# Performance work log

Hardware: AMD Instinct MI355X
Metric: run time of the kernel (lower is better)

## Reference

```python
import jax, jax.numpy as jnp
import numpy as np

D = 768  # input_hidden_dim
H = 768  # TGLU_hidden_dim
E = 128  # num_entity
B = 32   # batch_size
S = 128  # max_seq_len
LN_EPS = 1e-5


def setup_inputs() -> dict:
    key = jax.random.key(0)
    ks = jax.random.split(key, 14)
    sc = 1.0 / np.sqrt(D)
    return {
        "entity_text_cls": jax.random.normal(ks[0], (E, D), jnp.float32),
        "entity_text_tokens": jax.random.normal(ks[1], (E, S, D), jnp.float32),
        "mention_text_cls": jax.random.normal(ks[2], (B, D), jnp.float32),
        "mention_text_tokens": jax.random.normal(ks[3], (B, S, D), jnp.float32),
        "Wq": jax.random.normal(ks[4], (D, H), jnp.float32) * sc,
        "bq": jax.random.normal(ks[5], (H,), jnp.float32) * 0.02,
        "Wk": jax.random.normal(ks[6], (D, H), jnp.float32) * sc,
        "bk": jax.random.normal(ks[7], (H,), jnp.float32) * 0.02,
        "Wv": jax.random.normal(ks[8], (D, H), jnp.float32) * sc,
        "bv": jax.random.normal(ks[9], (H,), jnp.float32) * 0.02,
        "Wc": jax.random.normal(ks[10], (D, H), jnp.float32) * sc,
        "bc": jax.random.normal(ks[11], (H,), jnp.float32) * 0.02,
        "ln_g": jnp.ones((H,), jnp.float32),
        "ln_b": jnp.zeros((H,), jnp.float32),
    }


def reference(entity_text_cls, entity_text_tokens, mention_text_cls, mention_text_tokens,
              Wq, bq, Wk, bk, Wv, bv, Wc, bc, ln_g, ln_b):
    # projections
    cls_fc = entity_text_cls @ Wc + bc                     # [E, H]
    q = entity_text_tokens @ Wq + bq                       # [E, S, H]
    k = mention_text_tokens @ Wk + bk                      # [B, S, H]
    v = mention_text_tokens @ Wv + bv                      # [B, S, H]
    # broadcast cross attention: every entity attends to every mention
    scale = 1.0 / jnp.sqrt(jnp.asarray(H, q.dtype))
    scores = jnp.einsum('esh,bth->ebst', q, k) * scale     # [E, B, S, S]
    probs = jax.nn.softmax(scores, axis=-1)                # [E, B, S, S]
    # context = mean over query positions of probs @ v  -> fuse mean into einsum
    seq = jnp.asarray(q.shape[1], q.dtype)
    ctx = jnp.einsum('ebst,bth->ebh', probs, v) / seq      # [E, B, H]
    # layernorm over H
    mu = jnp.mean(ctx, axis=-1, keepdims=True)
    var = jnp.mean(jnp.square(ctx - mu), axis=-1, keepdims=True)
    ctx_ln = (ctx - mu) * jax.lax.rsqrt(var + LN_EPS) * ln_g + ln_b
    # dual matching scores
    g2l = jnp.einsum('eh,ebh->eb', cls_fc, ctx_ln).T       # [B, E]
    g2g = mention_text_cls @ entity_text_cls.T             # [B, E]
    return (g2l + g2g) * 0.5
```

## Files before the change

### kernel.cpp

```cpp
#include <hip/hip_runtime.h>

typedef unsigned short u16;
typedef __bf16 bf16x8 __attribute__((ext_vector_type(8)));
typedef float f32x4 __attribute__((ext_vector_type(4)));
typedef u16 u16x8 __attribute__((ext_vector_type(8)));
typedef u16 u16x4 __attribute__((ext_vector_type(4)));

static __device__ __forceinline__ u16 f2bf(float x){
  unsigned u = __float_as_uint(x);
  u += 0x7fffu + ((u >> 16) & 1u);
  return (u16)(u >> 16);
}
static __device__ __forceinline__ float bf2f(u16 u){
  return __uint_as_float(((unsigned)u) << 16);
}

#define MFMA __builtin_amdgcn_mfma_f32_16x16x32_bf16

__global__ __launch_bounds__(256) void prep(
    const float* __restrict__ s0, u16* __restrict__ d0,
    const float* __restrict__ s1, u16* __restrict__ d1,
    const float* __restrict__ s2, u16* __restrict__ d2,
    const float* __restrict__ s3, u16* __restrict__ d3,
    const float* __restrict__ w0, const float* __restrict__ w1,
    const float* __restrict__ w2, u16* __restrict__ e0,
    u16* __restrict__ e1, u16* __restrict__ e2)
{
  int blk = blockIdx.x;
  if (blk < 8016){
    int i = blk * 256 + threadIdx.x;
    const float* s; u16* d; int off;
    if (i < 1572864)      { s=s0; d=d0; off=i; }
    else if (i < 1966080) { s=s1; d=d1; off=i-1572864; }
    else if (i < 1978368) { s=s2; d=d2; off=i-1966080; }
    else                  { s=s3; d=d3; off=i-1978368; }
    const float4* s4 = (const float4*)s;
    float4 a = s4[(size_t)off*2], b = s4[(size_t)off*2+1];
    u16x8 r;
    r[0]=f2bf(a.x); r[1]=f2bf(a.y); r[2]=f2bf(a.z); r[3]=f2bf(a.w);
    r[4]=f2bf(b.x); r[5]=f2bf(b.y); r[6]=f2bf(b.z); r[7]=f2bf(b.w);
    *(u16x8*)(d + (size_t)off*8) = r;
  } else {
    int n = blk - 8016;
    int z = n / 576, rem = n % 576;
    const float* s = (z==0) ? w0 : (z==1) ? w1 : w2;
    u16*         d = (z==0) ? e0 : (z==1) ? e1 : e2;
    __shared__ float t[32][33];
    int bx = (rem % 24) * 32, by = (rem / 24) * 32;
    int tx = threadIdx.x & 31, ty = (threadIdx.x >> 5) * 4;
    for (int i=0;i<4;i++)
      t[ty+i][tx] = s[(size_t)(by+ty+i)*768 + bx+tx];
    __syncthreads();
    for (int i=0;i<4;i++)
      d[(size_t)(bx+ty+i)*768 + by+tx] = f2bf(t[tx][ty+i]);
  }
}

#define DECL_ACC \
  f32x4 acc00={},acc01={},acc02={},acc03={}, \
        acc10={},acc11={},acc12={},acc13={}, \
        acc20={},acc21={},acc22={},acc23={}, \
        acc30={},acc31={},acc32={},acc33={};

#define GLD1(GP, LP) __builtin_amdgcn_global_load_lds( \
    (const __attribute__((address_space(1))) unsigned int*)(GP), \
    (__attribute__((address_space(3))) unsigned int*)(LP), 16, 0, 0)

#define CORE_SETUP \
  int tid = threadIdx.x; \
  int lane = tid & 63, w = tid >> 6; \
  int wm = (w >> 1) * 64, wn = (w & 1) * 64; \
  int quad = lane >> 4, l16 = lane & 15; \
  int r8 = lane >> 3, c8 = lane & 7; \
  int p0 = quad ^ (l16 & 7); \
  const u16* Agl = Ablk + (size_t)(w*32 + r8)*KS + (size_t)((c8 ^ r8)*8); \
  const u16* Bgl = Bblk + (size_t)(w*32 + r8)*KS + (size_t)((c8 ^ r8)*8); \
  u16* sAl = sA + w*2048; \
  u16* sBl = sB + w*2048; \
  const u16* paA0 = sA + (wm + l16)*64 + p0*8; \
  const u16* paA1 = sA + (wm + l16)*64 + (p0^4)*8; \
  const u16* paB0 = sB + (wn + l16)*64 + p0*8; \
  const u16* paB1 = sB + (wn + l16)*64 + (p0^4)*8;

#define GLDS8(K0) do { \
  const u16* ga_ = Agl + (K0); \
  const u16* gb_ = Bgl + (K0); \
  GLD1(ga_,         sAl);        GLD1(ga_ +  8*KS, sAl +  512); \
  GLD1(ga_ + 16*KS, sAl + 1024); GLD1(ga_ + 24*KS, sAl + 1536); \
  GLD1(gb_,         sBl);        GLD1(gb_ +  8*KS, sBl +  512); \
  GLD1(gb_ + 16*KS, sBl + 1024); GLD1(gb_ + 24*KS, sBl + 1536); \
} while(0)

#define KKSTEP(PA, PB) do { \
  bf16x8 a0 = *(const bf16x8*)(PA); \
  bf16x8 a1 = *(const bf16x8*)((PA) + 1024); \
  bf16x8 a2 = *(const bf16x8*)((PA) + 2048); \
  bf16x8 a3 = *(const bf16x8*)((PA) + 3072); \
  bf16x8 b0 = *(const bf16x8*)(PB); \
  bf16x8 b1 = *(const bf16x8*)((PB) + 1024); \
  bf16x8 b2 = *(const bf16x8*)((PB) + 2048); \
  bf16x8 b3 = *(const bf16x8*)((PB) + 3072); \
  acc00 = MFMA(a0,b0,acc00,0,0,0); acc01 = MFMA(a0,b1,acc01,0,0,0); \
  acc02 = MFMA(a0,b2,acc02,0,0,0); acc03 = MFMA(a0,b3,acc03,0,0,0); \
  acc10 = MFMA(a1,b0,acc10,0,0,0); acc11 = MFMA(a1,b1,acc11,0,0,0); \
  acc12 = MFMA(a1,b2,acc12,0,0,0); acc13 = MFMA(a1,b3,acc13,0,0,0); \
  acc20 = MFMA(a2,b0,acc20,0,0,0); acc21 = MFMA(a2,b1,acc21,0,0,0); \
  acc22 = MFMA(a2,b2,acc22,0,0,0); acc23 = MFMA(a2,b3,acc23,0,0,0); \
  acc30 = MFMA(a3,b0,acc30,0,0,0); acc31 = MFMA(a3,b1,acc31,0,0,0); \
  acc32 = MFMA(a3,b2,acc32,0,0,0); acc33 = MFMA(a3,b3,acc33,0,0,0); \
} while(0)

#define KLOOP do { \
  for (int k0 = 0; k0 < KLEN; k0 += 64){ \
    __syncthreads(); \
    GLDS8(k0); \
    __syncthreads(); \
    KKSTEP(paA0, paB0); \
    KKSTEP(paA1, paB1); \
  } } while(0)

template<int KLEN, int KS, bool TRANSC>
static __device__ __forceinline__ void gemm128_core(
    const u16* __restrict__ Ablk, const u16* __restrict__ Bblk,
    const float* __restrict__ bias, u16* __restrict__ C,
    int mb, int nb, u16* sA, u16* sB)
{
  CORE_SETUP
  DECL_ACC
  KLOOP;
  int cb = nb*128 + wn + l16;
  float bb0=0.f, bb1=0.f, bb2=0.f, bb3=0.f;
  if (bias){ bb0=bias[cb]; bb1=bias[cb+16]; bb2=bias[cb+32]; bb3=bias[cb+48]; }
  if constexpr (!TRANSC) {
#define GEPI(IM,A0,A1,A2,A3) do { \
  int r0_ = mb*128 + wm + (IM)*16 + quad*4; \
  _Pragma("unroll") \
  for (int j=0;j<4;j++){ \
    C[(size_t)(r0_+j)*768 + cb     ] = f2bf(A0[j]+bb0); \
    C[(size_t)(r0_+j)*768 + cb + 16] = f2bf(A1[j]+bb1); \
    C[(size_t)(r0_+j)*768 + cb + 32] = f2bf(A2[j]+bb2); \
    C[(size_t)(r0_+j)*768 + cb + 48] = f2bf(A3[j]+bb3); \
  } } while(0)
    GEPI(0, acc00,acc01,acc02,acc03);
    GEPI(1, acc10,acc11,acc12,acc13);
    GEPI(2, acc20,acc21,acc22,acc23);
    GEPI(3, acc30,acc31,acc32,acc33);
#undef GEPI
  } else {
#define GEPT(IM,A0,A1,A2,A3) do { \
  int t0_ = wm + (IM)*16 + quad*4; \
  u16x4 p0 = {f2bf(A0[0]+bb0),f2bf(A0[1]+bb0),f2bf(A0[2]+bb0),f2bf(A0[3]+bb0)}; \
  u16x4 p1 = {f2bf(A1[0]+bb1),f2bf(A1[1]+bb1),f2bf(A1[2]+bb1),f2bf(A1[3]+bb1)}; \
  u16x4 p2 = {f2bf(A2[0]+bb2),f2bf(A2[1]+bb2),f2bf(A2[2]+bb2),f2bf(A2[3]+bb2)}; \
  u16x4 p3 = {f2bf(A3[0]+bb3),f2bf(A3[1]+bb3),f2bf(A3[2]+bb3),f2bf(A3[3]+bb3)}; \
  *(u16x4*)(C + (size_t)(cb     )*128 + t0_) = p0; \
  *(u16x4*)(C + (size_t)(cb + 16)*128 + t0_) = p1; \
  *(u16x4*)(C + (size_t)(cb + 32)*128 + t0_) = p2; \
  *(u16x4*)(C + (size_t)(cb + 48)*128 + t0_) = p3; \
} while(0)
    GEPT(0, acc00,acc01,acc02,acc03);
    GEPT(1, acc10,acc11,acc12,acc13);
    GEPT(2, acc20,acc21,acc22,acc23);
    GEPT(3, acc30,acc31,acc32,acc33);
#undef GEPT
  }
}

__global__ __launch_bounds__(256, 1) void gemm_kvc(
    const u16* __restrict__ men, const u16* __restrict__ eclsb,
    const u16* __restrict__ wkt, const u16* __restrict__ wvt,
    const u16* __restrict__ wct,
    const float* __restrict__ bk, const float* __restrict__ bv,
    const float* __restrict__ bc,
    u16* __restrict__ k2b, u16* __restrict__ vtb, u16* __restrict__ clsb)
{
  __shared__ __align__(16) u16 sA[128*64];
  __shared__ __align__(16) u16 sB[128*64];
  int y = blockIdx.y, mb = blockIdx.x;
  if (y < 6){
    gemm128_core<768,768,false>(men + (size_t)mb*128*768, wkt + (size_t)y*128*768,
                                bk, k2b, mb, y, sA, sB);
  } else if (y < 12){
    gemm128_core<768,768,true>(men + (size_t)mb*128*768, wvt + (size_t)(y-6)*128*768,
                               bv, vtb + (size_t)mb*98304, mb, y-6, sA, sB);
  } else {
    if (mb >= 6) return;
    gemm128_core<768,768,false>(eclsb, wct + (size_t)mb*128*768, bc, clsb, 0, mb, sA, sB);
  }
}

__global__ __launch_bounds__(256, 1) void gemm_g(
    const u16* __restrict__ k2b, const u16* __restrict__ wqb,
    const float* __restrict__ bq, u16* __restrict__ gtb,
    float* __restrict__ rbias)
{
  __shared__ __align__(16) u16 sA[128*64];
  __shared__ __align__(16) u16 sB[128*64];
  int y = blockIdx.y, mb = blockIdx.x;
  if (y < 6){
    gemm128_core<768,768,false>(k2b + (size_t)mb*128*768,
                                wqb + (size_t)y*128*768,
                                nullptr, gtb, mb, y, sA, sB);
  } else {
    int tid = threadIdx.x;
    int rr = tid >> 1, half = (tid & 1) * 384;
    int row = mb*128 + rr;
    const u16* p = k2b + (size_t)row*768 + half;
    const float* q = bq + half;
    float s = 0.f;
    #pragma unroll
    for (int i=0;i<48;i++){
      u16x8 v = *(const u16x8*)(p + i*8);
      s += bf2f(v[0])*q[i*8]   + bf2f(v[1])*q[i*8+1]
         + bf2f(v[2])*q[i*8+2] + bf2f(v[3])*q[i*8+3]
         + bf2f(v[4])*q[i*8+4] + bf2f(v[5])*q[i*8+5]
         + bf2f(v[6])*q[i*8+6] + bf2f(v[7])*q[i*8+7];
    }
    s += __shfl_xor(s, 1);
    if ((tid & 1) == 0) rbias[row] = s;
  }
}

__global__ __launch_bounds__(256, 1) void ctx2(
    const u16* __restrict__ ptbf, const u16* __restrict__ vtb,
    u16* __restrict__ ctxb)
{
  __shared__ __align__(16) u16 sA[128*64];
  __shared__ __align__(16) u16 sB[128*64];
  int b = blockIdx.y, nb = blockIdx.x;
  gemm128_core<128,128,false>(ptbf + (size_t)b*16384,
                              vtb + (size_t)b*98304 + (size_t)nb*16384,
                              nullptr, ctxb + (size_t)b*98304, 0, nb, sA, sB);
}

__global__ __launch_bounds__(256, 1) void attnk(
    const u16* __restrict__ ent, const u16* __restrict__ gt,
    const float* __restrict__ rbias, u16* __restrict__ ptbf)
{
  __shared__ __align__(16) u16 sA[128*64];
  __shared__ __align__(16) u16 sB[128*64];
  __shared__ float rbufA[256];
  __shared__ float rbufB[256];
  int bi = blockIdx.x;
  int b = bi >> 7, e = bi & 127;
  const u16* Ablk = ent + (size_t)e * 128 * 768;
  const u16* Bblk = gt  + (size_t)b * 128 * 768;
  constexpr int KLEN = 768, KS = 768;
  CORE_SETUP
  DECL_ACC
  KLOOP;
  const float c1 = 0.036084391824351615f * 1.4426950408889634f;
  float rs0 = rbias[b*128 + wn      + l16] * c1;
  float rs1 = rbias[b*128 + wn + 16 + l16] * c1;
  float rs2 = rbias[b*128 + wn + 32 + l16] * c1;
  float rs3 = rbias[b*128 + wn + 48 + l16] * c1;
#define EXPSUM(IM,A0,A1,A2,A3) do { \
  _Pragma("unroll") \
  for (int j=0;j<4;j++){ \
    int r_ = wm + (IM)*16 + quad*4 + j; \
    float e0 = exp2f(fmaf(A0[j], c1, rs0)); \
    float e1 = exp2f(fmaf(A1[j], c1, rs1)); \
    float e2 = exp2f(fmaf(A2[j], c1, rs2)); \
    float e3 = exp2f(fmaf(A3[j], c1, rs3)); \
    A0[j]=e0; A1[j]=e1; A2[j]=e2; A3[j]=e3; \
    float s = (e0+e1)+(e2+e3); \
    s += __shfl_xor(s,1); s += __shfl_xor(s,2); \
    s += __shfl_xor(s,4); s += __shfl_xor(s,8); \
    if (l16==0) rbufB[(w&1)*128 + r_] = s; \
  } } while(0)
  EXPSUM(0, acc00,acc01,acc02,acc03);
  EXPSUM(1, acc10,acc11,acc12,acc13);
  EXPSUM(2, acc20,acc21,acc22,acc23);
  EXPSUM(3, acc30,acc31,acc32,acc33);
#undef EXPSUM
  __syncthreads();
  float csum0=0.f, csum1=0.f, csum2=0.f, csum3=0.f;
#define CSUM(IM,A0,A1,A2,A3) do { \
  _Pragma("unroll") \
  for (int j=0;j<4;j++){ \
    int r_ = wm + (IM)*16 + quad*4 + j; \
    float inv = __builtin_amdgcn_rcpf(rbufB[r_]+rbufB[128+r_]); \
    csum0 += A0[j]*inv; csum1 += A1[j]*inv; \
    csum2 += A2[j]*inv; csum3 += A3[j]*inv; \
  } } while(0)
  CSUM(0, acc00,acc01,acc02,acc03);
  CSUM(1, acc10,acc11,acc12,acc13);
  CSUM(2, acc20,acc21,acc22,acc23);
  CSUM(3, acc30,acc31,acc32,acc33);
#undef CSUM
  csum0 += __shfl_xor(csum0,16); csum0 += __shfl_xor(csum0,32);
  csum1 += __shfl_xor(csum1,16); csum1 += __shfl_xor(csum1,32);
  csum2 += __shfl_xor(csum2,16); csum2 += __shfl_xor(csum2,32);
  csum3 += __shfl_xor(csum3,16); csum3 += __shfl_xor(csum3,32);
  if (quad == 0){
    rbufA[(w>>1)*128 + wn      + l16] = csum0;
    rbufA[(w>>1)*128 + wn + 16 + l16] = csum1;
    rbufA[(w>>1)*128 + wn + 32 + l16] = csum2;
    rbufA[(w>>1)*128 + wn + 48 + l16] = csum3;
  }
  __syncthreads();
  if (tid < 128)
    ptbf[((size_t)b*128 + e)*128 + tid] =
        f2bf((rbufA[tid] + rbufA[128+tid]) * 0.0078125f);
}

__global__ __launch_bounds__(256) void fin(
    const u16* __restrict__ ctxb, const u16* __restrict__ clsfc,
    const float* __restrict__ ecls, const float* __restrict__ mcls,
    const float* __restrict__ lng, const float* __restrict__ lnb,
    float* __restrict__ out)
{
  int bi = blockIdx.x;
  int b = bi >> 7, e = bi & 127;
  int tid = threadIdx.x;
  int lane = tid & 63, w = tid >> 6;
  __shared__ float redbuf[8];
  const u16* cr = ctxb + ((size_t)b*128 + e)*768;
  float a0 = bf2f(cr[tid]), a1 = bf2f(cr[tid+256]), a2 = bf2f(cr[tid+512]);
  float s1 = a0+a1+a2;
  float s2 = a0*a0 + a1*a1 + a2*a2;
  #pragma unroll
  for (int d2=1; d2<64; d2<<=1){ s1 += __shfl_xor(s1,d2); s2 += __shfl_xor(s2,d2); }
  if (lane==0){ redbuf[w]=s1; redbuf[4+w]=s2; }
  __syncthreads();
  s1 = redbuf[0]+redbuf[1]+redbuf[2]+redbuf[3];
  s2 = redbuf[4]+redbuf[5]+redbuf[6]+redbuf[7];
  float mu = s1 * (1.0f/768.0f);
  float var = s2 * (1.0f/768.0f) - mu*mu;
  float rstd = rsqrtf(var + 1e-5f);
  float dd = 0.f;
  {
    int h = tid;
    float y = (a0-mu)*rstd*lng[h] + lnb[h];
    dd += y * bf2f(clsfc[e*768+h]) + mcls[b*768+h]*ecls[e*768+h];
    h = tid + 256;
    y = (a1-mu)*rstd*lng[h] + lnb[h];
    dd += y * bf2f(clsfc[e*768+h]) + mcls[b*768+h]*ecls[e*768+h];
    h = tid + 512;
    y = (a2-mu)*rstd*lng[h] + lnb[h];
    dd += y * bf2f(clsfc[e*768+h]) + mcls[b*768+h]*ecls[e*768+h];
  }
  #pragma unroll
  for (int d2=1; d2<64; d2<<=1) dd += __shfl_xor(dd,d2);
  __syncthreads();
  if (lane==0) redbuf[w] = dd;
  __syncthreads();
  if (tid==0) out[bi] = 0.5f * (redbuf[0]+redbuf[1]+redbuf[2]+redbuf[3]);
}

extern "C" void kernel_launch(void* const* d_in, const int* in_sizes, int n_in,
                              void* d_out, int out_size, void* d_ws, size_t ws_size,
                              hipStream_t stream)
{
  (void)in_sizes; (void)n_in; (void)out_size; (void)ws_size;
  const float* ecls = (const float*)d_in[0];
  const float* etok = (const float*)d_in[1];
  const float* mcls = (const float*)d_in[2];
  const float* mtok = (const float*)d_in[3];
  const float* Wq   = (const float*)d_in[4];
  const float* bq   = (const float*)d_in[5];
  const float* Wk   = (const float*)d_in[6];
  const float* bk   = (const float*)d_in[7];
  const float* Wv   = (const float*)d_in[8];
  const float* bv   = (const float*)d_in[9];
  const float* Wc   = (const float*)d_in[10];
  const float* bc   = (const float*)d_in[11];
  const float* lng  = (const float*)d_in[12];
  const float* lnb  = (const float*)d_in[13];
  float* out = (float*)d_out;
  char* ws = (char*)d_ws;

  u16* ent_bf  = (u16*)(ws + 0);
  u16* men_bf  = (u16*)(ws + 25165824);
  u16* ecls_bf = (u16*)(ws + 31457280);
  u16* wq_bf   = (u16*)(ws + 31653888);
  u16* wkt     = (u16*)(ws + 32833536);
  u16* wvt     = (u16*)(ws + 34013184);
  u16* wct     = (u16*)(ws + 35192832);
  u16* k2b     = (u16*)(ws + 36372480);
  u16* vtb     = (u16*)(ws + 42663936);
  u16* clsb    = (u16*)(ws + 48955392);
  u16* gtb     = (u16*)(ws + 49152000);
  float* rbias = (float*)(ws + 55443456);
  u16* ptbf    = (u16*)(ws + 55459840);
  u16* ctxb    = (u16*)(ws + 56508416);

  prep<<<9744, 256, 0, stream>>>(etok, ent_bf, mtok, men_bf,
                                 ecls, ecls_bf, Wq, wq_bf,
                                 Wk, Wv, Wc, wkt, wvt, wct);
  gemm_kvc<<<dim3(32,13), 256, 0, stream>>>(men_bf, ecls_bf, wkt, wvt, wct,
                                            bk, bv, bc, k2b, vtb, clsb);
  gemm_g<<<dim3(32,7), 256, 0, stream>>>(k2b, wq_bf, bq, gtb, rbias);
  attnk<<<4096, 256, 0, stream>>>(ent_bf, gtb, rbias, ptbf);
  ctx2<<<dim3(6,32), 256, 0, stream>>>(ptbf, vtb, ctxb);
  fin<<<4096, 256, 0, stream>>>(ctxb, clsb, ecls, mcls, lng, lnb, out);
}
```

Measured before the change: 304.9 us.

## Precompute Wk·WqT product to drop K projection, widen attention tile

Folds the Q/K projections algebraically. A small 768x768 product M = Wq·Wkᵀ is computed in the prep kernel, so the mention-side G = men·Mᵀ + bias is built in one GEMM, and the separate K GEMM and its launch go away. The row-bias terms are rewritten as precomputed weight-bias dot products. The attention kernel now processes 256 entity rows (two entities) per block against 128 mention positions. It normalises softmax per row with in-register shuffles instead of shared-memory round trips, halving the grid. This adds register pressure (32 accumulators per wave) and a bf16 rounding of the fused weight product.

```diff
diff --git a/kernel.cpp b/kernel.cpp
--- a/kernel.cpp
+++ b/kernel.cpp
@@ -17,54 +17,15 @@
 
 #define MFMA __builtin_amdgcn_mfma_f32_16x16x32_bf16
 
-__global__ __launch_bounds__(256) void prep(
-    const float* __restrict__ s0, u16* __restrict__ d0,
-    const float* __restrict__ s1, u16* __restrict__ d1,
-    const float* __restrict__ s2, u16* __restrict__ d2,
-    const float* __restrict__ s3, u16* __restrict__ d3,
-    const float* __restrict__ w0, const float* __restrict__ w1,
-    const float* __restrict__ w2, u16* __restrict__ e0,
-    u16* __restrict__ e1, u16* __restrict__ e2)
-{
-  int blk = blockIdx.x;
-  if (blk < 8016){
-    int i = blk * 256 + threadIdx.x;
-    const float* s; u16* d; int off;
-    if (i < 1572864)      { s=s0; d=d0; off=i; }
-    else if (i < 1966080) { s=s1; d=d1; off=i-1572864; }
-    else if (i < 1978368) { s=s2; d=d2; off=i-1966080; }
-    else                  { s=s3; d=d3; off=i-1978368; }
-    const float4* s4 = (const float4*)s;
-    float4 a = s4[(size_t)off*2], b = s4[(size_t)off*2+1];
-    u16x8 r;
-    r[0]=f2bf(a.x); r[1]=f2bf(a.y); r[2]=f2bf(a.z); r[3]=f2bf(a.w);
-    r[4]=f2bf(b.x); r[5]=f2bf(b.y); r[6]=f2bf(b.z); r[7]=f2bf(b.w);
-    *(u16x8*)(d + (size_t)off*8) = r;
-  } else {
-    int n = blk - 8016;
-    int z = n / 576, rem = n % 576;
-    const float* s = (z==0) ? w0 : (z==1) ? w1 : w2;
-    u16*         d = (z==0) ? e0 : (z==1) ? e1 : e2;
-    __shared__ float t[32][33];
-    int bx = (rem % 24) * 32, by = (rem / 24) * 32;
-    int tx = threadIdx.x & 31, ty = (threadIdx.x >> 5) * 4;
-    for (int i=0;i<4;i++)
-      t[ty+i][tx] = s[(size_t)(by+ty+i)*768 + bx+tx];
-    __syncthreads();
-    for (int i=0;i<4;i++)
-      d[(size_t)(bx+ty+i)*768 + by+tx] = f2bf(t[tx][ty+i]);
-  }
-}
+#define GLD1(GP, LP) __builtin_amdgcn_global_load_lds( \
+    (const __attribute__((address_space(1))) unsigned int*)(GP), \
+    (__attribute__((address_space(3))) unsigned int*)(LP), 16, 0, 0)
 
 #define DECL_ACC \
   f32x4 acc00={},acc01={},acc02={},acc03={}, \
         acc10={},acc11={},acc12={},acc13={}, \
         acc20={},acc21={},acc22={},acc23={}, \
         acc30={},acc31={},acc32={},acc33={};
-
-#define GLD1(GP, LP) __builtin_amdgcn_global_load_lds( \
-    (const __attribute__((address_space(1))) unsigned int*)(GP), \
-    (__attribute__((address_space(3))) unsigned int*)(LP), 16, 0, 0)
 
 #define CORE_SETUP \
   int tid = threadIdx.x; \
@@ -149,14 +110,14 @@
   } else {
 #define GEPT(IM,A0,A1,A2,A3) do { \
   int t0_ = wm + (IM)*16 + quad*4; \
-  u16x4 p0 = {f2bf(A0[0]+bb0),f2bf(A0[1]+bb0),f2bf(A0[2]+bb0),f2bf(A0[3]+bb0)}; \
-  u16x4 p1 = {f2bf(A1[0]+bb1),f2bf(A1[1]+bb1),f2bf(A1[2]+bb1),f2bf(A1[3]+bb1)}; \
-  u16x4 p2 = {f2bf(A2[0]+bb2),f2bf(A2[1]+bb2),f2bf(A2[2]+bb2),f2bf(A2[3]+bb2)}; \
-  u16x4 p3 = {f2bf(A3[0]+bb3),f2bf(A3[1]+bb3),f2bf(A3[2]+bb3),f2bf(A3[3]+bb3)}; \
-  *(u16x4*)(C + (size_t)(cb     )*128 + t0_) = p0; \
-  *(u16x4*)(C + (size_t)(cb + 16)*128 + t0_) = p1; \
-  *(u16x4*)(C + (size_t)(cb + 32)*128 + t0_) = p2; \
-  *(u16x4*)(C + (size_t)(cb + 48)*128 + t0_) = p3; \
+  u16x4 p0_ = {f2bf(A0[0]+bb0),f2bf(A0[1]+bb0),f2bf(A0[2]+bb0),f2bf(A0[3]+bb0)}; \
+  u16x4 p1_ = {f2bf(A1[0]+bb1),f2bf(A1[1]+bb1),f2bf(A1[2]+bb1),f2bf(A1[3]+bb1)}; \
+  u16x4 p2_ = {f2bf(A2[0]+bb2),f2bf(A2[1]+bb2),f2bf(A2[2]+bb2),f2bf(A2[3]+bb2)}; \
+  u16x4 p3_ = {f2bf(A3[0]+bb3),f2bf(A3[1]+bb3),f2bf(A3[2]+bb3),f2bf(A3[3]+bb3)}; \
+  *(u16x4*)(C + (size_t)(cb     )*128 + t0_) = p0_; \
+  *(u16x4*)(C + (size_t)(cb + 16)*128 + t0_) = p1_; \
+  *(u16x4*)(C + (size_t)(cb + 32)*128 + t0_) = p2_; \
+  *(u16x4*)(C + (size_t)(cb + 48)*128 + t0_) = p3_; \
 } while(0)
     GEPT(0, acc00,acc01,acc02,acc03);
     GEPT(1, acc10,acc11,acc12,acc13);
@@ -166,49 +127,162 @@
   }
 }
 
-__global__ __launch_bounds__(256, 1) void gemm_kvc(
+__global__ __launch_bounds__(256) void prep(
+    const float* __restrict__ etok, u16* __restrict__ entb,
+    const float* __restrict__ mtok, u16* __restrict__ menb,
+    const float* __restrict__ ecls, u16* __restrict__ eclsb,
+    const float* __restrict__ Wv, const float* __restrict__ Wc,
+    u16* __restrict__ wvt, u16* __restrict__ wct,
+    const float* __restrict__ Wq, const float* __restrict__ Wk,
+    u16* __restrict__ mtb,
+    const float* __restrict__ bq, const float* __restrict__ bk,
+    float* __restrict__ wrb, float* __restrict__ c2b)
+{
+  __shared__ __align__(16) u16 shm[2*128*72];
+  int blk = blockIdx.x;
+  int tid = threadIdx.x;
+  if (blk < 7728){
+    int i = blk * 256 + tid;
+    const float* s; u16* d; int off;
+    if (i < 1572864)      { s=etok; d=entb; off=i; }
+    else if (i < 1966080) { s=mtok; d=menb; off=i-1572864; }
+    else                  { s=ecls; d=eclsb; off=i-1966080; }
+    const float4* s4 = (const float4*)s;
+    float4 a = s4[(size_t)off*2], b = s4[(size_t)off*2+1];
+    u16x8 r;
+    r[0]=f2bf(a.x); r[1]=f2bf(a.y); r[2]=f2bf(a.z); r[3]=f2bf(a.w);
+    r[4]=f2bf(b.x); r[5]=f2bf(b.y); r[6]=f2bf(b.z); r[7]=f2bf(b.w);
+    *(u16x8*)(d + (size_t)off*8) = r;
+  } else if (blk < 8880){
+    int n = blk - 7728;
+    int z = n / 576, rem = n % 576;
+    const float* s = z ? Wc : Wv;
+    u16*         d = z ? wct : wvt;
+    float* t = (float*)shm;
+    int bx = (rem % 24) * 32, by = (rem / 24) * 32;
+    int tx = tid & 31, ty = (tid >> 5) * 4;
+    for (int i=0;i<4;i++)
+      t[(ty+i)*33 + tx] = s[(size_t)(by+ty+i)*768 + bx+tx];
+    __syncthreads();
+    for (int i=0;i<4;i++)
+      d[(size_t)(bx+ty+i)*768 + by+tx] = f2bf(t[tx*33 + ty+i]);
+  } else if (blk < 8916){
+    int n = blk - 8880; int mbq = n/6, nbq = n%6;
+    u16* tA = shm; u16* tB = shm + 128*72;
+    int lane = tid & 63, w = tid >> 6;
+    int wm = (w >> 1) * 64, wn = (w & 1) * 64;
+    int quad = lane >> 4, l16 = lane & 15;
+    int sr = tid >> 3, sc = (tid & 7) * 8;
+    const float* Ag = Wq + (size_t)(mbq*128+sr)*768 + sc;
+    const float* Bg = Wk + (size_t)(nbq*128+sr)*768 + sc;
+    u16* tAp = tA + sr*72 + sc;
+    u16* tBp = tB + sr*72 + sc;
+    DECL_ACC
+    for (int k0=0;k0<768;k0+=64){
+      __syncthreads();
+#define STG(G) do { \
+      float4 xa0=*(const float4*)(Ag+(G)*32*768+k0), xa1=*(const float4*)(Ag+(G)*32*768+k0+4); \
+      float4 xb0=*(const float4*)(Bg+(G)*32*768+k0), xb1=*(const float4*)(Bg+(G)*32*768+k0+4); \
+      u16x8 ra={f2bf(xa0.x),f2bf(xa0.y),f2bf(xa0.z),f2bf(xa0.w), \
+                f2bf(xa1.x),f2bf(xa1.y),f2bf(xa1.z),f2bf(xa1.w)}; \
+      u16x8 rb={f2bf(xb0.x),f2bf(xb0.y),f2bf(xb0.z),f2bf(xb0.w), \
+                f2bf(xb1.x),f2bf(xb1.y),f2bf(xb1.z),f2bf(xb1.w)}; \
+      *(u16x8*)(tAp+(G)*32*72)=ra; *(u16x8*)(tBp+(G)*32*72)=rb; \
+      } while(0)
+      STG(0); STG(1); STG(2); STG(3);
+#undef STG
+      __syncthreads();
+#define KK72(KB) do { \
+      const u16* pa_=tA+(wm+l16)*72+(KB)+quad*8; \
+      const u16* pb_=tB+(wn+l16)*72+(KB)+quad*8; \
+      bf16x8 a0=*(const bf16x8*)(pa_),      a1=*(const bf16x8*)(pa_+16*72); \
+      bf16x8 a2=*(const bf16x8*)(pa_+32*72),a3=*(const bf16x8*)(pa_+48*72); \
+      bf16x8 b0=*(const bf16x8*)(pb_),      b1=*(const bf16x8*)(pb_+16*72); \
+      bf16x8 b2=*(const bf16x8*)(pb_+32*72),b3=*(const bf16x8*)(pb_+48*72); \
+      acc00=MFMA(a0,b0,acc00,0,0,0); acc01=MFMA(a0,b1,acc01,0,0,0); \
+      acc02=MFMA(a0,b2,acc02,0,0,0); acc03=MFMA(a0,b3,acc03,0,0,0); \
+      acc10=MFMA(a1,b0,acc10,0,0,0); acc11=MFMA(a1,b1,acc11,0,0,0); \
+      acc12=MFMA(a1,b2,acc12,0,0,0); acc13=MFMA(a1,b3,acc13,0,0,0); \
+      acc20=MFMA(a2,b0,acc20,0,0,0); acc21=MFMA(a2,b1,acc21,0,0,0); \
+      acc22=MFMA(a2,b2,acc22,0,0,0); acc23=MFMA(a2,b3,acc23,0,0,0); \
+      acc30=MFMA(a3,b0,acc30,0,0,0); acc31=MFMA(a3,b1,acc31,0,0,0); \
+      acc32=MFMA(a3,b2,acc32,0,0,0); acc33=MFMA(a3,b3,acc33,0,0,0); \
+      } while(0)
+      KK72(0); KK72(32);
+#undef KK72
+    }
+    int cb = nbq*128 + wn + l16;
+#define GEPM(IM,A0,A1,A2,A3) do { \
+    int r0_ = mbq*128 + wm + (IM)*16 + quad*4; \
+    _Pragma("unroll") \
+    for (int j=0;j<4;j++){ \
+      mtb[(size_t)(r0_+j)*768 + cb     ] = f2bf(A0[j]); \
+      mtb[(size_t)(r0_+j)*768 + cb + 16] = f2bf(A1[j]); \
+      mtb[(size_t)(r0_+j)*768 + cb + 32] = f2bf(A2[j]); \
+      mtb[(size_t)(r0_+j)*768 + cb + 48] = f2bf(A3[j]); \
+    } } while(0)
+    GEPM(0, acc00,acc01,acc02,acc03);
+    GEPM(1, acc10,acc11,acc12,acc13);
+    GEPM(2, acc20,acc21,acc22,acc23);
+    GEPM(3, acc30,acc31,acc32,acc33);
+#undef GEPM
+  } else if (blk < 8928){
+    int n = blk - 8916;
+    const float* M; const float* v; float* o;
+    int j;
+    if (n < 6){ M=Wk; v=bq; o=wrb; j=n; } else { M=Wq; v=bk; o=c2b; j=n-6; }
+    int rr = tid >> 1, row = j*128 + rr;
+    const float4* p = (const float4*)(M + (size_t)row*768 + (tid&1)*384);
+    const float4* q = (const float4*)(v + (tid&1)*384);
+    float s = 0.f;
+    #pragma unroll 8
+    for (int i=0;i<96;i++){
+      float4 a=p[i], c=q[i];
+      s += a.x*c.x + a.y*c.y + a.z*c.z + a.w*c.w;
+    }
+    s += __shfl_xor(s, 1);
+    if (!(tid&1)) o[row] = s;
+  } else {
+    float s = 0.f;
+    for (int i=tid;i<768;i+=256) s += bk[i]*bq[i];
+    #pragma unroll
+    for (int d2=1; d2<64; d2<<=1) s += __shfl_xor(s,d2);
+    float* red = (float*)shm;
+    int lane = tid & 63, w = tid >> 6;
+    if (lane==0) red[w]=s;
+    __syncthreads();
+    if (tid==0) wrb[768] = red[0]+red[1]+red[2]+red[3];
+  }
+}
+
+__global__ __launch_bounds__(256, 1) void proj(
     const u16* __restrict__ men, const u16* __restrict__ eclsb,
-    const u16* __restrict__ wkt, const u16* __restrict__ wvt,
-    const u16* __restrict__ wct,
-    const float* __restrict__ bk, const float* __restrict__ bv,
-    const float* __restrict__ bc,
-    u16* __restrict__ k2b, u16* __restrict__ vtb, u16* __restrict__ clsb)
+    const u16* __restrict__ wvt, const u16* __restrict__ wct,
+    const u16* __restrict__ mtb,
+    const float* __restrict__ bv, const float* __restrict__ bc,
+    const float* __restrict__ c2b, const float* __restrict__ wrb,
+    u16* __restrict__ vtb, u16* __restrict__ gtb, u16* __restrict__ clsb,
+    float* __restrict__ rbias)
 {
   __shared__ __align__(16) u16 sA[128*64];
   __shared__ __align__(16) u16 sB[128*64];
   int y = blockIdx.y, mb = blockIdx.x;
   if (y < 6){
-    gemm128_core<768,768,false>(men + (size_t)mb*128*768, wkt + (size_t)y*128*768,
-                                bk, k2b, mb, y, sA, sB);
+    gemm128_core<768,768,true>(men + (size_t)mb*128*768, wvt + (size_t)y*128*768,
+                               bv, vtb + (size_t)mb*98304, mb, y, sA, sB);
   } else if (y < 12){
-    gemm128_core<768,768,true>(men + (size_t)mb*128*768, wvt + (size_t)(y-6)*128*768,
-                               bv, vtb + (size_t)mb*98304, mb, y-6, sA, sB);
-  } else {
+    gemm128_core<768,768,false>(men + (size_t)mb*128*768, mtb + (size_t)(y-6)*128*768,
+                                c2b, gtb, mb, y-6, sA, sB);
+  } else if (y == 12){
     if (mb >= 6) return;
     gemm128_core<768,768,false>(eclsb, wct + (size_t)mb*128*768, bc, clsb, 0, mb, sA, sB);
-  }
-}
-
-__global__ __launch_bounds__(256, 1) void gemm_g(
-    const u16* __restrict__ k2b, const u16* __restrict__ wqb,
-    const float* __restrict__ bq, u16* __restrict__ gtb,
-    float* __restrict__ rbias)
-{
-  __shared__ __align__(16) u16 sA[128*64];
-  __shared__ __align__(16) u16 sB[128*64];
-  int y = blockIdx.y, mb = blockIdx.x;
-  if (y < 6){
-    gemm128_core<768,768,false>(k2b + (size_t)mb*128*768,
-                                wqb + (size_t)y*128*768,
-                                nullptr, gtb, mb, y, sA, sB);
   } else {
     int tid = threadIdx.x;
-    int rr = tid >> 1, half = (tid & 1) * 384;
-    int row = mb*128 + rr;
-    const u16* p = k2b + (size_t)row*768 + half;
-    const float* q = bq + half;
+    int rr = tid >> 1, row = mb*128 + rr;
+    const u16* p = men + (size_t)row*768 + (tid&1)*384;
+    const float* q = wrb + (tid&1)*384;
     float s = 0.f;
-    #pragma unroll
+    #pragma unroll 8
     for (int i=0;i<48;i++){
       u16x8 v = *(const u16x8*)(p + i*8);
       s += bf2f(v[0])*q[i*8]   + bf2f(v[1])*q[i*8+1]
@@ -217,7 +291,145 @@
          + bf2f(v[6])*q[i*8+6] + bf2f(v[7])*q[i*8+7];
     }
     s += __shfl_xor(s, 1);
-    if ((tid & 1) == 0) rbias[row] = s;
+    if (!(tid&1)) rbias[row] = s + wrb[768];
+  }
+}
+
+__global__ __launch_bounds__(256, 1) void attnk(
+    const u16* __restrict__ ent, const u16* __restrict__ gt,
+    const float* __restrict__ rbias, u16* __restrict__ ptbf)
+{
+  __shared__ __align__(16) u16 sA[256*64];
+  __shared__ __align__(16) u16 sB[128*64];
+  __shared__ float rbuf[512];
+  int bi = blockIdx.x;
+  int b = bi >> 6, ep = bi & 63;
+  const u16* Ablk = ent + (size_t)ep * 256 * 768;
+  const u16* Bblk = gt  + (size_t)b * 128 * 768;
+  int tid = threadIdx.x;
+  int lane = tid & 63, w = tid >> 6;
+  int quad = lane >> 4, l16 = lane & 15;
+  int r8 = lane >> 3, c8 = lane & 7;
+  int p0 = quad ^ (l16 & 7);
+  const u16* Agl = Ablk + (size_t)(w*64 + r8)*768 + (size_t)((c8 ^ r8)*8);
+  const u16* Bgl = Bblk + (size_t)(w*32 + r8)*768 + (size_t)((c8 ^ r8)*8);
+  u16* sAl = sA + w*4096;
+  u16* sBl = sB + w*2048;
+  const u16* paA0 = sA + (w*64 + l16)*64 + p0*8;
+  const u16* paA1 = sA + (w*64 + l16)*64 + (p0^4)*8;
+  const u16* paB0 = sB + l16*64 + p0*8;
+  const u16* paB1 = sB + l16*64 + (p0^4)*8;
+  f32x4 acc00={},acc01={},acc02={},acc03={},acc04={},acc05={},acc06={},acc07={},
+        acc10={},acc11={},acc12={},acc13={},acc14={},acc15={},acc16={},acc17={},
+        acc20={},acc21={},acc22={},acc23={},acc24={},acc25={},acc26={},acc27={},
+        acc30={},acc31={},acc32={},acc33={},acc34={},acc35={},acc36={},acc37={};
+#define AKH(PA, PB) do { \
+  bf16x8 b0 = *(const bf16x8*)(PB); \
+  bf16x8 b1 = *(const bf16x8*)((PB) + 1024); \
+  bf16x8 b2 = *(const bf16x8*)((PB) + 2048); \
+  bf16x8 b3 = *(const bf16x8*)((PB) + 3072); \
+  bf16x8 b4 = *(const bf16x8*)((PB) + 4096); \
+  bf16x8 b5 = *(const bf16x8*)((PB) + 5120); \
+  bf16x8 b6 = *(const bf16x8*)((PB) + 6144); \
+  bf16x8 b7 = *(const bf16x8*)((PB) + 7168); \
+  bf16x8 a_; \
+  a_ = *(const bf16x8*)(PA); \
+  acc00=MFMA(a_,b0,acc00,0,0,0); acc01=MFMA(a_,b1,acc01,0,0,0); \
+  acc02=MFMA(a_,b2,acc02,0,0,0); acc03=MFMA(a_,b3,acc03,0,0,0); \
+  acc04=MFMA(a_,b4,acc04,0,0,0); acc05=MFMA(a_,b5,acc05,0,0,0); \
+  acc06=MFMA(a_,b6,acc06,0,0,0); acc07=MFMA(a_,b7,acc07,0,0,0); \
+  a_ = *(const bf16x8*)((PA) + 1024); \
+  acc10=MFMA(a_,b0,acc10,0,0,0); acc11=MFMA(a_,b1,acc11,0,0,0); \
+  acc12=MFMA(a_,b2,acc12,0,0,0); acc13=MFMA(a_,b3,acc13,0,0,0); \
+  acc14=MFMA(a_,b4,acc14,0,0,0); acc15=MFMA(a_,b5,acc15,0,0,0); \
+  acc16=MFMA(a_,b6,acc16,0,0,0); acc17=MFMA(a_,b7,acc17,0,0,0); \
+  a_ = *(const bf16x8*)((PA) + 2048); \
+  acc20=MFMA(a_,b0,acc20,0,0,0); acc21=MFMA(a_,b1,acc21,0,0,0); \
+  acc22=MFMA(a_,b2,acc22,0,0,0); acc23=MFMA(a_,b3,acc23,0,0,0); \
+  acc24=MFMA(a_,b4,acc24,0,0,0); acc25=MFMA(a_,b5,acc25,0,0,0); \
+  acc26=MFMA(a_,b6,acc26,0,0,0); acc27=MFMA(a_,b7,acc27,0,0,0); \
+  a_ = *(const bf16x8*)((PA) + 3072); \
+  acc30=MFMA(a_,b0,acc30,0,0,0); acc31=MFMA(a_,b1,acc31,0,0,0); \
+  acc32=MFMA(a_,b2,acc32,0,0,0); acc33=MFMA(a_,b3,acc33,0,0,0); \
+  acc34=MFMA(a_,b4,acc34,0,0,0); acc35=MFMA(a_,b5,acc35,0,0,0); \
+  acc36=MFMA(a_,b6,acc36,0,0,0); acc37=MFMA(a_,b7,acc37,0,0,0); \
+} while(0)
+  for (int k0 = 0; k0 < 768; k0 += 64){
+    __syncthreads();
+    {
+      const u16* ga_ = Agl + k0;
+      const u16* gb_ = Bgl + k0;
+      GLD1(ga_,          sAl);        GLD1(ga_ +  8*768, sAl +  512);
+      GLD1(ga_ + 16*768, sAl + 1024); GLD1(ga_ + 24*768, sAl + 1536);
+      GLD1(ga_ + 32*768, sAl + 2048); GLD1(ga_ + 40*768, sAl + 2560);
+      GLD1(ga_ + 48*768, sAl + 3072); GLD1(ga_ + 56*768, sAl + 3584);
+      GLD1(gb_,          sBl);        GLD1(gb_ +  8*768, sBl +  512);
+      GLD1(gb_ + 16*768, sBl + 1024); GLD1(gb_ + 24*768, sBl + 1536);
+    }
+    __syncthreads();
+    AKH(paA0, paB0);
+    AKH(paA1, paB1);
+  }
+#undef AKH
+  const float c1 = 0.036084391824351615f * 1.4426950408889634f;
+  float rs0 = rbias[b*128        + l16] * c1;
+  float rs1 = rbias[b*128 +  16  + l16] * c1;
+  float rs2 = rbias[b*128 +  32  + l16] * c1;
+  float rs3 = rbias[b*128 +  48  + l16] * c1;
+  float rs4 = rbias[b*128 +  64  + l16] * c1;
+  float rs5 = rbias[b*128 +  80  + l16] * c1;
+  float rs6 = rbias[b*128 +  96  + l16] * c1;
+  float rs7 = rbias[b*128 + 112  + l16] * c1;
+  float cs0=0.f,cs1=0.f,cs2=0.f,cs3=0.f,cs4=0.f,cs5=0.f,cs6=0.f,cs7=0.f;
+#define EXPROW(A0,A1,A2,A3,A4,A5,A6,A7) do { \
+  _Pragma("unroll") \
+  for (int j=0;j<4;j++){ \
+    float e0 = exp2f(fmaf(A0[j], c1, rs0)); \
+    float e1 = exp2f(fmaf(A1[j], c1, rs1)); \
+    float e2 = exp2f(fmaf(A2[j], c1, rs2)); \
+    float e3 = exp2f(fmaf(A3[j], c1, rs3)); \
+    float e4 = exp2f(fmaf(A4[j], c1, rs4)); \
+    float e5 = exp2f(fmaf(A5[j], c1, rs5)); \
+    float e6 = exp2f(fmaf(A6[j], c1, rs6)); \
+    float e7 = exp2f(fmaf(A7[j], c1, rs7)); \
+    float s_ = ((e0+e1)+(e2+e3)) + ((e4+e5)+(e6+e7)); \
+    s_ += __shfl_xor(s_,1); s_ += __shfl_xor(s_,2); \
+    s_ += __shfl_xor(s_,4); s_ += __shfl_xor(s_,8); \
+    float inv = __builtin_amdgcn_rcpf(s_); \
+    cs0 = fmaf(e0,inv,cs0); cs1 = fmaf(e1,inv,cs1); \
+    cs2 = fmaf(e2,inv,cs2); cs3 = fmaf(e3,inv,cs3); \
+    cs4 = fmaf(e4,inv,cs4); cs5 = fmaf(e5,inv,cs5); \
+    cs6 = fmaf(e6,inv,cs6); cs7 = fmaf(e7,inv,cs7); \
+  } } while(0)
+  EXPROW(acc00,acc01,acc02,acc03,acc04,acc05,acc06,acc07);
+  EXPROW(acc10,acc11,acc12,acc13,acc14,acc15,acc16,acc17);
+  EXPROW(acc20,acc21,acc22,acc23,acc24,acc25,acc26,acc27);
+  EXPROW(acc30,acc31,acc32,acc33,acc34,acc35,acc36,acc37);
+#undef EXPROW
+  cs0 += __shfl_xor(cs0,16); cs0 += __shfl_xor(cs0,32);
+  cs1 += __shfl_xor(cs1,16); cs1 += __shfl_xor(cs1,32);
+  cs2 += __shfl_xor(cs2,16); cs2 += __shfl_xor(cs2,32);
+  cs3 += __shfl_xor(cs3,16); cs3 += __shfl_xor(cs3,32);
+  cs4 += __shfl_xor(cs4,16); cs4 += __shfl_xor(cs4,32);
+  cs5 += __shfl_xor(cs5,16); cs5 += __shfl_xor(cs5,32);
+  cs6 += __shfl_xor(cs6,16); cs6 += __shfl_xor(cs6,32);
+  cs7 += __shfl_xor(cs7,16); cs7 += __shfl_xor(cs7,32);
+  if (quad == 0){
+    rbuf[w*128        + l16] = cs0;
+    rbuf[w*128 +  16  + l16] = cs1;
+    rbuf[w*128 +  32  + l16] = cs2;
+    rbuf[w*128 +  48  + l16] = cs3;
+    rbuf[w*128 +  64  + l16] = cs4;
+    rbuf[w*128 +  80  + l16] = cs5;
+    rbuf[w*128 +  96  + l16] = cs6;
+    rbuf[w*128 + 112  + l16] = cs7;
+  }
+  __syncthreads();
+  {
+    int half = tid >> 7, t = tid & 127;
+    float v = rbuf[half*256 + t] + rbuf[half*256 + 128 + t];
+    int e = ep*2 + half;
+    ptbf[((size_t)b*128 + e)*128 + t] = f2bf(v * 0.0078125f);
   }
 }
 
@@ -231,77 +443,6 @@
   gemm128_core<128,128,false>(ptbf + (size_t)b*16384,
                               vtb + (size_t)b*98304 + (size_t)nb*16384,
                               nullptr, ctxb + (size_t)b*98304, 0, nb, sA, sB);
-}
-
-__global__ __launch_bounds__(256, 1) void attnk(
-    const u16* __restrict__ ent, const u16* __restrict__ gt,
-    const float* __restrict__ rbias, u16* __restrict__ ptbf)
-{
-  __shared__ __align__(16) u16 sA[128*64];
-  __shared__ __align__(16) u16 sB[128*64];
-  __shared__ float rbufA[256];
-  __shared__ float rbufB[256];
-  int bi = blockIdx.x;
-  int b = bi >> 7, e = bi & 127;
-  const u16* Ablk = ent + (size_t)e * 128 * 768;
-  const u16* Bblk = gt  + (size_t)b * 128 * 768;
-  constexpr int KLEN = 768, KS = 768;
-  CORE_SETUP
-  DECL_ACC
-  KLOOP;
-  const float c1 = 0.036084391824351615f * 1.4426950408889634f;
-  float rs0 = rbias[b*128 + wn      + l16] * c1;
-  float rs1 = rbias[b*128 + wn + 16 + l16] * c1;
-  float rs2 = rbias[b*128 + wn + 32 + l16] * c1;
-  float rs3 = rbias[b*128 + wn + 48 + l16] * c1;
-#define EXPSUM(IM,A0,A1,A2,A3) do { \
-  _Pragma("unroll") \
-  for (int j=0;j<4;j++){ \
-    int r_ = wm + (IM)*16 + quad*4 + j; \
-    float e0 = exp2f(fmaf(A0[j], c1, rs0)); \
-    float e1 = exp2f(fmaf(A1[j], c1, rs1)); \
-    float e2 = exp2f(fmaf(A2[j], c1, rs2)); \
-    float e3 = exp2f(fmaf(A3[j], c1, rs3)); \
-    A0[j]=e0; A1[j]=e1; A2[j]=e2; A3[j]=e3; \
-    float s = (e0+e1)+(e2+e3); \
-    s += __shfl_xor(s,1); s += __shfl_xor(s,2); \
-    s += __shfl_xor(s,4); s += __shfl_xor(s,8); \
-    if (l16==0) rbufB[(w&1)*128 + r_] = s; \
-  } } while(0)
-  EXPSUM(0, acc00,acc01,acc02,acc03);
-  EXPSUM(1, acc10,acc11,acc12,acc13);
-  EXPSUM(2, acc20,acc21,acc22,acc23);
-  EXPSUM(3, acc30,acc31,acc32,acc33);
-#undef EXPSUM
-  __syncthreads();
-  float csum0=0.f, csum1=0.f, csum2=0.f, csum3=0.f;
-#define CSUM(IM,A0,A1,A2,A3) do { \
-  _Pragma("unroll") \
-  for (int j=0;j<4;j++){ \
-    int r_ = wm + (IM)*16 + quad*4 + j; \
-    float inv = __builtin_amdgcn_rcpf(rbufB[r_]+rbufB[128+r_]); \
-    csum0 += A0[j]*inv; csum1 += A1[j]*inv; \
-    csum2 += A2[j]*inv; csum3 += A3[j]*inv; \
-  } } while(0)
-  CSUM(0, acc00,acc01,acc02,acc03);
-  CSUM(1, acc10,acc11,acc12,acc13);
-  CSUM(2, acc20,acc21,acc22,acc23);
-  CSUM(3, acc30,acc31,acc32,acc33);
-#undef CSUM
-  csum0 += __shfl_xor(csum0,16); csum0 += __shfl_xor(csum0,32);
-  csum1 += __shfl_xor(csum1,16); csum1 += __shfl_xor(csum1,32);
-  csum2 += __shfl_xor(csum2,16); csum2 += __shfl_xor(csum2,32);
-  csum3 += __shfl_xor(csum3,16); csum3 += __shfl_xor(csum3,32);
-  if (quad == 0){
-    rbufA[(w>>1)*128 + wn      + l16] = csum0;
-    rbufA[(w>>1)*128 + wn + 16 + l16] = csum1;
-    rbufA[(w>>1)*128 + wn + 32 + l16] = csum2;
-    rbufA[(w>>1)*128 + wn + 48 + l16] = csum3;
-  }
-  __syncthreads();
-  if (tid < 128)
-    ptbf[((size_t)b*128 + e)*128 + tid] =
-        f2bf((rbufA[tid] + rbufA[128+tid]) * 0.0078125f);
 }
 
 __global__ __launch_bounds__(256) void fin(
@@ -373,25 +514,25 @@
   u16* ent_bf  = (u16*)(ws + 0);
   u16* men_bf  = (u16*)(ws + 25165824);
   u16* ecls_bf = (u16*)(ws + 31457280);
-  u16* wq_bf   = (u16*)(ws + 31653888);
-  u16* wkt     = (u16*)(ws + 32833536);
-  u16* wvt     = (u16*)(ws + 34013184);
-  u16* wct     = (u16*)(ws + 35192832);
-  u16* k2b     = (u16*)(ws + 36372480);
-  u16* vtb     = (u16*)(ws + 42663936);
-  u16* clsb    = (u16*)(ws + 48955392);
-  u16* gtb     = (u16*)(ws + 49152000);
-  float* rbias = (float*)(ws + 55443456);
-  u16* ptbf    = (u16*)(ws + 55459840);
-  u16* ctxb    = (u16*)(ws + 56508416);
-
-  prep<<<9744, 256, 0, stream>>>(etok, ent_bf, mtok, men_bf,
-                                 ecls, ecls_bf, Wq, wq_bf,
-                                 Wk, Wv, Wc, wkt, wvt, wct);
-  gemm_kvc<<<dim3(32,13), 256, 0, stream>>>(men_bf, ecls_bf, wkt, wvt, wct,
-                                            bk, bv, bc, k2b, vtb, clsb);
-  gemm_g<<<dim3(32,7), 256, 0, stream>>>(k2b, wq_bf, bq, gtb, rbias);
-  attnk<<<4096, 256, 0, stream>>>(ent_bf, gtb, rbias, ptbf);
+  u16* wvt     = (u16*)(ws + 31653888);
+  u16* wct     = (u16*)(ws + 32833536);
+  u16* mtb     = (u16*)(ws + 34013184);
+  u16* vtb     = (u16*)(ws + 35192832);
+  u16* clsb    = (u16*)(ws + 41484288);
+  u16* gtb     = (u16*)(ws + 41680896);
+  float* rbias = (float*)(ws + 47972352);
+  float* wrb   = (float*)(ws + 47988736);
+  float* c2b   = (float*)(ws + 47992832);
+  u16* ptbf    = (u16*)(ws + 47996928);
+  u16* ctxb    = (u16*)(ws + 49045504);
+
+  prep<<<8929, 256, 0, stream>>>(etok, ent_bf, mtok, men_bf, ecls, ecls_bf,
+                                 Wv, Wc, wvt, wct, Wq, Wk, mtb,
+                                 bq, bk, wrb, c2b);
+  proj<<<dim3(32,14), 256, 0, stream>>>(men_bf, ecls_bf, wvt, wct, mtb,
+                                        bv, bc, c2b, wrb,
+                                        vtb, gtb, clsb, rbias);
+  attnk<<<2048, 256, 0, stream>>>(ent_bf, gtb, rbias, ptbf);
   ctx2<<<dim3(6,32), 256, 0, stream>>>(ptbf, vtb, ctxb);
   fin<<<4096, 256, 0, stream>>>(ctxb, clsb, ecls, mcls, lng, lnb, out);
 }
```

After: 372.6 us. 22.2% more time.
